# Kernel tuning notes

Measured on AMD Instinct MI355X. Metric: run time of the kernel, lower is better.

The kernel has to match this reference:

```python
import jax, jax.numpy as jnp
import numpy as np
jax.config.update("jax_enable_x64", True)  # match torch int64 hash wraparound

K = 4096  # codebook size
HASH_C = jnp.int64(73244475)


def mueller_hash(x):
    x = (x >> 16 ^ x) * HASH_C
    x = (x >> 16 ^ x) * HASH_C
    return x >> 16 ^ x


def fourier_act(x):
    # sin on even feature indices, cos on odd
    even = (jnp.arange(x.shape[-1]) % 2) == 0
    return jnp.where(even, jnp.sin(x), jnp.cos(x))


def setup_inputs() -> dict:
    key = jax.random.key(0)
    ks = jax.random.split(key, 10)
    f32 = jnp.float32
    N, D, H = 8192, 1024, 4096
    s = 0.02
    return {
        "x": jax.random.normal(ks[0], (N, D), dtype=f32),
        "w1": jax.random.normal(ks[1], (H, D), dtype=f32) * s,
        "b1": jnp.zeros((H,), dtype=f32),
        "w2": jax.random.normal(ks[2], (H, 2 * H), dtype=f32) * s,
        "b2": jnp.zeros((H,), dtype=f32),
        "w3": jax.random.normal(ks[3], (H, H), dtype=f32) * s,
        "b3": jnp.zeros((H,), dtype=f32),
        "w4": jax.random.normal(ks[4], (D, H), dtype=f32) * s,
        "b4": jnp.zeros((D,), dtype=f32),
        "emb": jax.random.normal(ks[5], (K, D), dtype=f32),
    }


def reference(x, w1, b1, w2, b2, w3, b3, w4, b4, emb):
    # FourierMLP
    h = x @ w1.T + b1                                  # [N, H]
    h = jnp.concatenate([h, fourier_act(h)], axis=-1)  # [N, 2H] (FourierAct cat=True)
    h = fourier_act(h @ w2.T + b2)                     # [N, H]
    h = fourier_act(h @ w3.T + b3)                     # [N, H]
    z = h @ w4.T + b4                                  # [N, D]

    # latent: cdist argmin == squared-distance argmin
    z2 = jnp.sum(z * z, axis=-1, keepdims=True)        # [N, 1]
    e2 = jnp.sum(emb * emb, axis=-1)                   # [K]
    d2 = z2 - 2.0 * (z @ emb.T) + e2                   # [N, K]
    idx = jnp.argmin(d2, axis=-1).astype(jnp.int64)    # [N]

    quantized = jnp.zeros_like(z)
    for i in range(1, 4):
        sel = mueller_hash(idx + jnp.int64(i * K)) & jnp.int64(K - 1)  # % K (K pow2)
        quantized = quantized + emb[sel] / 3.0
    return quantized
```

## Files before the change

kernel.cpp:

```cpp
#include <hip/hip_runtime.h>
#include <cstdint>

constexpr int NB = 8192;
constexpr int Dd = 1024;
constexpr int Hh = 4096;
constexpr int Kc = 4096;

using ull = unsigned long long;
typedef _Float16 half8 __attribute__((ext_vector_type(8)));
typedef float floatx16 __attribute__((ext_vector_type(16)));

#define TPB 256

__device__ __forceinline__ float fourier1(int col, float v) {
    return (col & 1) ? __cosf(v) : __sinf(v);
}

#define ASYNC_CP16(gp, sp)                                                          \
    __builtin_amdgcn_global_load_lds(                                               \
        (const __attribute__((address_space(1))) unsigned int*)(gp),                \
        (__attribute__((address_space(3))) unsigned int*)(sp), 16, 0, 0)

template<int MODE>
__global__ __launch_bounds__(TPB, 2)
void gemm_split(const _Float16* __restrict__ Agh, const _Float16* __restrict__ Agl,
                const _Float16* __restrict__ Bgh, const _Float16* __restrict__ Bgl,
                const float* __restrict__ bias, float invscale,
                _Float16* __restrict__ Ch, _Float16* __restrict__ Cl,
                int Kd, int ldc,
                const float* __restrict__ e2, ull* __restrict__ gkey)
{
    __shared__ _Float16 sAh[128 * 32];
    __shared__ _Float16 sAl[128 * 32];
    __shared__ _Float16 sBh[256 * 32];
    __shared__ _Float16 sBl[256 * 32];
    __shared__ ull red[256];

    const int tid = threadIdx.x, lane = tid & 63;
    const int w = tid >> 6;
    const int bn = blockIdx.x, bm = blockIdx.y;
    const int wm = w >> 1, wn = w & 1;
    const int l31 = lane & 31, lh = lane >> 5;

    size_t aoff[2], boff[4];
#pragma unroll
    for (int s = 0; s < 2; ++s) {
        int q = s * 256 + tid; int r = q >> 2;
        int c = (q & 3) ^ ((r >> 1) & 3);
        aoff[s] = (size_t)(bm * 128 + r) * Kd + c * 8;
    }
#pragma unroll
    for (int s = 0; s < 4; ++s) {
        int q = s * 256 + tid; int r = q >> 2;
        int c = (q & 3) ^ ((r >> 1) & 3);
        boff[s] = (size_t)(bn * 256 + r) * Kd + c * 8;
    }

    int arow[2], asw[2], brow[4], bsw[4];
#pragma unroll
    for (int mt = 0; mt < 2; ++mt) {
        int r = wm * 64 + mt * 32 + l31; arow[mt] = r * 32; asw[mt] = (r >> 1) & 3;
    }
#pragma unroll
    for (int nt = 0; nt < 4; ++nt) {
        int r = wn * 128 + nt * 32 + l31; brow[nt] = r * 32; bsw[nt] = (r >> 1) & 3;
    }

    floatx16 acc[2][4];
#pragma unroll
    for (int mt = 0; mt < 2; ++mt)
#pragma unroll
        for (int nt = 0; nt < 4; ++nt)
#pragma unroll
            for (int i = 0; i < 16; ++i) acc[mt][nt][i] = 0.f;

    for (int k0 = 0; k0 < Kd; k0 += 32) {
#pragma unroll
        for (int s = 0; s < 2; ++s) {
            ASYNC_CP16(Agh + aoff[s] + k0, sAh + (s * 256 + tid) * 8);
            ASYNC_CP16(Agl + aoff[s] + k0, sAl + (s * 256 + tid) * 8);
        }
#pragma unroll
        for (int s = 0; s < 4; ++s) {
            ASYNC_CP16(Bgh + boff[s] + k0, sBh + (s * 256 + tid) * 8);
            ASYNC_CP16(Bgl + boff[s] + k0, sBl + (s * 256 + tid) * 8);
        }
        __syncthreads();

#pragma unroll
        for (int kk = 0; kk < 2; ++kk) {
            const int ck = kk * 2 + lh;
            half8 ah[2], al[2], bh[4], bl[4];
#pragma unroll
            for (int mt = 0; mt < 2; ++mt) {
                int off = arow[mt] + (ck ^ asw[mt]) * 8;
                ah[mt] = *(const half8*)(sAh + off);
                al[mt] = *(const half8*)(sAl + off);
            }
#pragma unroll
            for (int nt = 0; nt < 4; ++nt) {
                int off = brow[nt] + (ck ^ bsw[nt]) * 8;
                bh[nt] = *(const half8*)(sBh + off);
                bl[nt] = *(const half8*)(sBl + off);
            }
#pragma unroll
            for (int mt = 0; mt < 2; ++mt)
#pragma unroll
                for (int nt = 0; nt < 4; ++nt)
                    acc[mt][nt] = __builtin_amdgcn_mfma_f32_32x32x16_f16(ah[mt], bh[nt], acc[mt][nt], 0, 0, 0);
#pragma unroll
            for (int mt = 0; mt < 2; ++mt)
#pragma unroll
                for (int nt = 0; nt < 4; ++nt)
                    acc[mt][nt] = __builtin_amdgcn_mfma_f32_32x32x16_f16(ah[mt], bl[nt], acc[mt][nt], 0, 0, 0);
#pragma unroll
            for (int mt = 0; mt < 2; ++mt)
#pragma unroll
                for (int nt = 0; nt < 4; ++nt)
                    acc[mt][nt] = __builtin_amdgcn_mfma_f32_32x32x16_f16(al[mt], bh[nt], acc[mt][nt], 0, 0, 0);
        }
        __syncthreads();
    }

    if (MODE != 3) {
        float bs[4];
#pragma unroll
        for (int nt = 0; nt < 4; ++nt) bs[nt] = bias[bn * 256 + wn * 128 + nt * 32 + l31];
#pragma unroll
        for (int mt = 0; mt < 2; ++mt) {
#pragma unroll
            for (int nt = 0; nt < 4; ++nt) {
                const int col = bn * 256 + wn * 128 + nt * 32 + l31;
#pragma unroll
                for (int r = 0; r < 16; ++r) {
                    const int mrow = (r & 3) + 8 * (r >> 2) + 4 * lh;
                    const size_t row = (size_t)(bm * 128 + wm * 64 + mt * 32 + mrow);
                    const float v = acc[mt][nt][r] * invscale + bs[nt];
                    const size_t o = row * ldc + col;
                    if (MODE == 0) {
                        _Float16 h = (_Float16)v;
                        Ch[o] = h; Cl[o] = (_Float16)(v - (float)h);
                    } else if (MODE == 1) {
                        float f = fourier1(col, v);
                        _Float16 h = (_Float16)f;
                        Ch[o] = h; Cl[o] = (_Float16)(f - (float)h);
                    } else {
                        _Float16 h = (_Float16)v;
                        Ch[o] = h; Cl[o] = (_Float16)(v - (float)h);
                        float f = fourier1(col, v);
                        _Float16 hf = (_Float16)f;
                        Ch[o + Hh] = hf; Cl[o + Hh] = (_Float16)(f - (float)hf);
                    }
                }
            }
        }
    } else {
        float es[4];
#pragma unroll
        for (int nt = 0; nt < 4; ++nt) es[nt] = e2[bn * 256 + wn * 128 + nt * 32 + l31];
#pragma unroll
        for (int mt = 0; mt < 2; ++mt) {
#pragma unroll
            for (int r = 0; r < 16; ++r) {
                ull best = ~0ull;
#pragma unroll
                for (int nt = 0; nt < 4; ++nt) {
                    const int col = bn * 256 + wn * 128 + nt * 32 + l31;
                    float sc = es[nt] - 2.0f * acc[mt][nt][r];
                    unsigned u = __float_as_uint(sc);
                    u = (u & 0x80000000u) ? ~u : (u | 0x80000000u);
                    ull key = ((ull)u << 32) | (unsigned)col;
                    best = best < key ? best : key;
                }
#pragma unroll
                for (int m = 16; m >= 1; m >>= 1) {
                    ull o = __shfl_xor(best, m, 64);
                    best = best < o ? best : o;
                }
                if (l31 == 0) {
                    int rl = wm * 64 + mt * 32 + (r & 3) + 8 * (r >> 2) + 4 * lh;
                    red[rl * 2 + wn] = best;
                }
            }
        }
        __syncthreads();
        if (tid < 128) {
            ull a = red[tid * 2], b = red[tid * 2 + 1];
            atomicMin(&gkey[(size_t)bm * 128 + tid], a < b ? a : b);
        }
    }
}

__global__ void split_f16(const float* __restrict__ src, _Float16* __restrict__ hi,
                          _Float16* __restrict__ lo, int n8, float scale)
{
    int i = blockIdx.x * blockDim.x + threadIdx.x;
    if (i >= n8) return;
    const float4* s4 = (const float4*)src;
    float4 v0 = s4[i * 2], v1 = s4[i * 2 + 1];
    float v[8] = {v0.x, v0.y, v0.z, v0.w, v1.x, v1.y, v1.z, v1.w};
    half8 h, l;
#pragma unroll
    for (int j = 0; j < 8; ++j) {
        float x = v[j] * scale;
        _Float16 hh = (_Float16)x;
        h[j] = hh;
        l[j] = (_Float16)(x - (float)hh);
    }
    *(half8*)(hi + (size_t)i * 8) = h;
    *(half8*)(lo + (size_t)i * 8) = l;
}

__global__ void init_gkey(ull* gkey) {
    int i = blockIdx.x * blockDim.x + threadIdx.x;
    if (i < NB) gkey[i] = ~0ull;
}

__global__ void e2_kernel(const float* __restrict__ emb, float* __restrict__ e2) {
    int k = blockIdx.x, t = threadIdx.x;
    float s = 0.f;
    for (int d = t; d < Dd; d += 256) {
        float v = emb[(size_t)k * Dd + d];
        s += v * v;
    }
    __shared__ float r[256];
    r[t] = s; __syncthreads();
    for (int off = 128; off > 0; off >>= 1) {
        if (t < off) r[t] += r[t + off];
        __syncthreads();
    }
    if (t == 0) e2[k] = r[0];
}

__device__ __forceinline__ long long mueller(long long x) {
    x = (long long)((unsigned long long)(x ^ (x >> 16)) * 73244475ull);
    x = (long long)((unsigned long long)(x ^ (x >> 16)) * 73244475ull);
    return x ^ (x >> 16);
}

__global__ void out_kernel(const float* __restrict__ emb,
                           const ull* __restrict__ gkey,
                           float* __restrict__ out) {
    const int n = blockIdx.x;
    const int t = threadIdx.x;
    long long idx = (long long)(unsigned)(gkey[n] & 0xFFFFFFFFull);
    int s1 = (int)(mueller(idx + 1LL * Kc) & (long long)(Kc - 1));
    int s2 = (int)(mueller(idx + 2LL * Kc) & (long long)(Kc - 1));
    int s3 = (int)(mueller(idx + 3LL * Kc) & (long long)(Kc - 1));
    const float* e1p = emb + (size_t)s1 * Dd;
    const float* e2p = emb + (size_t)s2 * Dd;
    const float* e3p = emb + (size_t)s3 * Dd;
    float* op = out + (size_t)n * Dd;
    for (int d = t; d < Dd; d += 256)
        op[d] = e1p[d] / 3.0f + e2p[d] / 3.0f + e3p[d] / 3.0f;
}

__device__ __forceinline__ float fourier1p(int col, float v) {
    return (col & 1) ? cosf(v) : sinf(v);
}

template<int MODE>
__global__ __launch_bounds__(TPB)
void gemm_tn(const float* __restrict__ A, const float* __restrict__ B,
             const float* __restrict__ bias, float* __restrict__ C,
             int Kd, int ldc)
{
    __shared__ float As[16][132];
    __shared__ float Bs[16][132];
    const int t  = threadIdx.x;
    const int bn = blockIdx.x, bm = blockIdx.y;
    const int rowL = t >> 2;
    const int kq   = t & 3;
    const int rm   = (t >> 4) << 3;
    const int rn   = (t & 15) << 3;

    const float* Ab = A + (size_t)(bm * 128 + rowL) * Kd + kq * 4;
    const float* Bb = B + (size_t)(bn * 128 + rowL) * Kd + kq * 4;
    const size_t strideHalf = (size_t)64 * Kd;

    float acc[8][8];
#pragma unroll
    for (int i = 0; i < 8; ++i)
#pragma unroll
        for (int j = 0; j < 8; ++j) acc[i][j] = 0.f;

    for (int k0 = 0; k0 < Kd; k0 += 16) {
        float4 a0 = *(const float4*)(Ab + k0);
        float4 a1 = *(const float4*)(Ab + strideHalf + k0);
        float4 b0 = *(const float4*)(Bb + k0);
        float4 b1 = *(const float4*)(Bb + strideHalf + k0);
        __syncthreads();
        As[kq*4+0][rowL]    = a0.x; As[kq*4+1][rowL]    = a0.y;
        As[kq*4+2][rowL]    = a0.z; As[kq*4+3][rowL]    = a0.w;
        As[kq*4+0][rowL+64] = a1.x; As[kq*4+1][rowL+64] = a1.y;
        As[kq*4+2][rowL+64] = a1.z; As[kq*4+3][rowL+64] = a1.w;
        Bs[kq*4+0][rowL]    = b0.x; Bs[kq*4+1][rowL]    = b0.y;
        Bs[kq*4+2][rowL]    = b0.z; Bs[kq*4+3][rowL]    = b0.w;
        Bs[kq*4+0][rowL+64] = b1.x; Bs[kq*4+1][rowL+64] = b1.y;
        Bs[kq*4+2][rowL+64] = b1.z; Bs[kq*4+3][rowL+64] = b1.w;
        __syncthreads();
#pragma unroll
        for (int kk = 0; kk < 16; ++kk) {
            float4 av0 = *(const float4*)&As[kk][rm];
            float4 av1 = *(const float4*)&As[kk][rm + 4];
            float4 bv0 = *(const float4*)&Bs[kk][rn];
            float4 bv1 = *(const float4*)&Bs[kk][rn + 4];
            float a[8] = {av0.x, av0.y, av0.z, av0.w, av1.x, av1.y, av1.z, av1.w};
            float b[8] = {bv0.x, bv0.y, bv0.z, bv0.w, bv1.x, bv1.y, bv1.z, bv1.w};
#pragma unroll
            for (int i = 0; i < 8; ++i)
#pragma unroll
                for (int j = 0; j < 8; ++j)
                    acc[i][j] = fmaf(a[i], b[j], acc[i][j]);
        }
    }

    const int gm = bm * 128 + rm;
    const int gn = bn * 128 + rn;
#pragma unroll
    for (int i = 0; i < 8; ++i) {
#pragma unroll
        for (int j = 0; j < 8; ++j) {
            float v = acc[i][j] + bias[gn + j];
            size_t o = (size_t)(gm + i) * ldc + (gn + j);
            if (MODE == 0) {
                C[o] = v;
            } else if (MODE == 1) {
                C[o] = fourier1p(gn + j, v);
            } else {
                C[o]      = v;
                C[o + Hh] = fourier1p(gn + j, v);
            }
        }
    }
}

__global__ __launch_bounds__(TPB)
void dist_argmin(const float* __restrict__ Z, const float* __restrict__ E,
                 const float* __restrict__ e2, ull* __restrict__ gkey)
{
    __shared__ float As[16][132];
    __shared__ float Bs[16][132];
    __shared__ ull   red[128][16];
    const int t  = threadIdx.x;
    const int bn = blockIdx.x, bm = blockIdx.y;
    const int rowL = t >> 2;
    const int kq   = t & 3;
    const int rm   = (t >> 4) << 3;
    const int rn   = (t & 15) << 3;
    const int Kd = Dd;

    const float* Ab = Z + (size_t)(bm * 128 + rowL) * Kd + kq * 4;
    const float* Bb = E + (size_t)(bn * 128 + rowL) * Kd + kq * 4;
    const size_t strideHalf = (size_t)64 * Kd;

    float acc[8][8];
#pragma unroll
    for (int i = 0; i < 8; ++i)
#pragma unroll
        for (int j = 0; j < 8; ++j) acc[i][j] = 0.f;

    for (int k0 = 0; k0 < Kd; k0 += 16) {
        float4 a0 = *(const float4*)(Ab + k0);
        float4 a1 = *(const float4*)(Ab + strideHalf + k0);
        float4 b0 = *(const float4*)(Bb + k0);
        float4 b1 = *(const float4*)(Bb + strideHalf + k0);
        __syncthreads();
        As[kq*4+0][rowL]    = a0.x; As[kq*4+1][rowL]    = a0.y;
        As[kq*4+2][rowL]    = a0.z; As[kq*4+3][rowL]    = a0.w;
        As[kq*4+0][rowL+64] = a1.x; As[kq*4+1][rowL+64] = a1.y;
        As[kq*4+2][rowL+64] = a1.z; As[kq*4+3][rowL+64] = a1.w;
        Bs[kq*4+0][rowL]    = b0.x; Bs[kq*4+1][rowL]    = b0.y;
        Bs[kq*4+2][rowL]    = b0.z; Bs[kq*4+3][rowL]    = b0.w;
        Bs[kq*4+0][rowL+64] = b1.x; Bs[kq*4+1][rowL+64] = b1.y;
        Bs[kq*4+2][rowL+64] = b1.z; Bs[kq*4+3][rowL+64] = b1.w;
        __syncthreads();
#pragma unroll
        for (int kk = 0; kk < 16; ++kk) {
            float4 av0 = *(const float4*)&As[kk][rm];
            float4 av1 = *(const float4*)&As[kk][rm + 4];
            float4 bv0 = *(const float4*)&Bs[kk][rn];
            float4 bv1 = *(const float4*)&Bs[kk][rn + 4];
            float a[8] = {av0.x, av0.y, av0.z, av0.w, av1.x, av1.y, av1.z, av1.w};
            float b[8] = {bv0.x, bv0.y, bv0.z, bv0.w, bv1.x, bv1.y, bv1.z, bv1.w};
#pragma unroll
            for (int i = 0; i < 8; ++i)
#pragma unroll
                for (int j = 0; j < 8; ++j)
                    acc[i][j] = fmaf(a[i], b[j], acc[i][j]);
        }
    }

    const int gn = bn * 128 + rn;
#pragma unroll
    for (int i = 0; i < 8; ++i) {
        ull best = ~0ull;
#pragma unroll
        for (int j = 0; j < 8; ++j) {
            int gk = gn + j;
            float sc = e2[gk] - 2.0f * acc[i][j];
            unsigned u = __float_as_uint(sc);
            u = (u & 0x80000000u) ? ~u : (u | 0x80000000u);
            ull key = ((ull)u << 32) | (unsigned)gk;
            best = best < key ? best : key;
        }
        red[rm + i][t & 15] = best;
    }
    __syncthreads();
    if (t < 128) {
        ull m = red[t][0];
#pragma unroll
        for (int q = 1; q < 16; ++q) m = m < red[t][q] ? m : red[t][q];
        atomicMin(&gkey[(size_t)bm * 128 + t], m);
    }
}

extern "C" void kernel_launch(void* const* d_in, const int* in_sizes, int n_in,
                              void* d_out, int out_size, void* d_ws, size_t ws_size,
                              hipStream_t stream) {
    const float* x   = (const float*)d_in[0];
    const float* w1  = (const float*)d_in[1];
    const float* b1  = (const float*)d_in[2];
    const float* w2  = (const float*)d_in[3];
    const float* b2  = (const float*)d_in[4];
    const float* w3  = (const float*)d_in[5];
    const float* b3  = (const float*)d_in[6];
    const float* w4  = (const float*)d_in[7];
    const float* b4  = (const float*)d_in[8];
    const float* emb = (const float*)d_in[9];
    float* out = (float*)d_out;

    const size_t MB = 1024 * 1024;

    if (ws_size >= 512 * MB) {
        char* W = (char*)d_ws;
        _Float16* hcat_h = (_Float16*)(W);
        _Float16* hcat_l = (_Float16*)(W + 128 * MB);
        _Float16* w3h = (_Float16*)(W);
        _Float16* w3l = (_Float16*)(W + 32 * MB);
        _Float16* w4h = (_Float16*)(W + 64 * MB);
        _Float16* w4l = (_Float16*)(W + 72 * MB);
        _Float16* eh  = (_Float16*)(W + 80 * MB);
        _Float16* el  = (_Float16*)(W + 88 * MB);
        float*    e2b = (float*)   (W + 96 * MB);
        ull*      gkey = (ull*)    (W + 96 * MB + 16 * 1024);
        _Float16* w2h = (_Float16*)(W + 256 * MB);
        _Float16* w2l = (_Float16*)(W + 320 * MB);
        _Float16* h3h = (_Float16*)(W + 256 * MB);
        _Float16* h3l = (_Float16*)(W + 320 * MB);
        _Float16* xh  = (_Float16*)(W + 384 * MB);
        _Float16* xl  = (_Float16*)(W + 400 * MB);
        _Float16* w1h = (_Float16*)(W + 416 * MB);
        _Float16* w1l = (_Float16*)(W + 424 * MB);
        _Float16* h2h = (_Float16*)(W + 384 * MB);
        _Float16* h2l = (_Float16*)(W + 448 * MB);
        _Float16* zh  = (_Float16*)d_out;
        _Float16* zl  = zh + (size_t)NB * Dd;

        const float WS = 64.0f, IWS = 1.0f / 64.0f;

        split_f16<<<dim3(1048576 / 256), 256, 0, stream>>>(x,  xh,  xl,  1048576, 1.0f);
        split_f16<<<dim3(524288  / 256), 256, 0, stream>>>(w1, w1h, w1l, 524288,  WS);
        split_f16<<<dim3(4194304 / 256), 256, 0, stream>>>(w2, w2h, w2l, 4194304, WS);

        gemm_split<2><<<dim3(Hh / 256, NB / 128), TPB, 0, stream>>>(
            xh, xl, w1h, w1l, b1, IWS, hcat_h, hcat_l, Dd, 2 * Hh, nullptr, nullptr);
        gemm_split<1><<<dim3(Hh / 256, NB / 128), TPB, 0, stream>>>(
            hcat_h, hcat_l, w2h, w2l, b2, IWS, h2h, h2l, 2 * Hh, Hh, nullptr, nullptr);

        split_f16<<<dim3(2097152 / 256), 256, 0, stream>>>(w3,  w3h, w3l, 2097152, WS);
        split_f16<<<dim3(524288  / 256), 256, 0, stream>>>(w4,  w4h, w4l, 524288,  WS);
        split_f16<<<dim3(524288  / 256), 256, 0, stream>>>(emb, eh,  el,  524288,  1.0f);
        e2_kernel<<<dim3(Kc), dim3(256), 0, stream>>>(emb, e2b);
        init_gkey<<<dim3(NB / 256), dim3(256), 0, stream>>>(gkey);

        gemm_split<1><<<dim3(Hh / 256, NB / 128), TPB, 0, stream>>>(
            h2h, h2l, w3h, w3l, b3, IWS, h3h, h3l, Hh, Hh, nullptr, nullptr);
        gemm_split<0><<<dim3(Dd / 256, NB / 128), TPB, 0, stream>>>(
            h3h, h3l, w4h, w4l, b4, IWS, zh, zl, Hh, Dd, nullptr, nullptr);
        gemm_split<3><<<dim3(Kc / 256, NB / 128), TPB, 0, stream>>>(
            zh, zl, eh, el, nullptr, 1.0f, nullptr, nullptr, Dd, 0, e2b, gkey);

        out_kernel<<<dim3(NB), dim3(256), 0, stream>>>(emb, gkey, out);
    } else {
        float* hcat  = (float*)d_ws;
        float* h2    = hcat + (size_t)NB * 2 * Hh;
        float* e2buf = h2 + (size_t)NB * Hh;
        ull*   gkey  = (ull*)(e2buf + Kc);
        float* h3    = hcat;

        init_gkey<<<dim3((NB + 255) / 256), dim3(256), 0, stream>>>(gkey);
        e2_kernel<<<dim3(Kc), dim3(256), 0, stream>>>(emb, e2buf);
        gemm_tn<2><<<dim3(Hh / 128, NB / 128), TPB, 0, stream>>>(x, w1, b1, hcat, Dd, 2 * Hh);
        gemm_tn<1><<<dim3(Hh / 128, NB / 128), TPB, 0, stream>>>(hcat, w2, b2, h2, 2 * Hh, Hh);
        gemm_tn<1><<<dim3(Hh / 128, NB / 128), TPB, 0, stream>>>(h2, w3, b3, h3, Hh, Hh);
        gemm_tn<0><<<dim3(Dd / 128, NB / 128), TPB, 0, stream>>>(h3, w4, b4, out, Hh, Dd);
        dist_argmin<<<dim3(Kc / 128, NB / 128), TPB, 0, stream>>>(out, emb, e2buf, gkey);
        out_kernel<<<dim3(NB), dim3(256), 0, stream>>>(emb, gkey, out);
    }
}
```

Before: 3.698 ms.

## Store GEMM A operand in MFMA fragment layout and load it directly to registers

Activations are now written by each GEMM epilogue, and by a new split kernel for x, in a pre-tiled layout that matches the 32x32x16 MFMA A-fragment order. The GEMM then reads A straight from global memory into registers with one contiguous 16-byte load per lane, dropping the A shared-memory tiles and their LDS reads. This is meant to cut LDS traffic and shared-memory footprint in the main loop. In exchange, the two waves that share an A tile each fetch it from global or L2 separately, and the A loads are not double-buffered, so their latency may be exposed.

```diff
diff --git a/kernel.cpp b/kernel.cpp
--- a/kernel.cpp
+++ b/kernel.cpp
@@ -20,6 +20,7 @@
     __builtin_amdgcn_global_load_lds(                                               \
         (const __attribute__((address_space(1))) unsigned int*)(gp),                \
         (__attribute__((address_space(3))) unsigned int*)(sp), 16, 0, 0)
+
 
 template<int MODE>
 __global__ __launch_bounds__(TPB, 2)
@@ -30,8 +31,6 @@
                 int Kd, int ldc,
                 const float* __restrict__ e2, ull* __restrict__ gkey)
 {
-    __shared__ _Float16 sAh[128 * 32];
-    __shared__ _Float16 sAl[128 * 32];
     __shared__ _Float16 sBh[256 * 32];
     __shared__ _Float16 sBl[256 * 32];
     __shared__ ull red[256];
@@ -41,14 +40,9 @@
     const int bn = blockIdx.x, bm = blockIdx.y;
     const int wm = w >> 1, wn = w & 1;
     const int l31 = lane & 31, lh = lane >> 5;
-
-    size_t aoff[2], boff[4];
-#pragma unroll
-    for (int s = 0; s < 2; ++s) {
-        int q = s * 256 + tid; int r = q >> 2;
-        int c = (q & 3) ^ ((r >> 1) & 3);
-        aoff[s] = (size_t)(bm * 128 + r) * Kd + c * 8;
-    }
+    const int kpf = Kd >> 4;
+
+    size_t boff[4];
 #pragma unroll
     for (int s = 0; s < 4; ++s) {
         int q = s * 256 + tid; int r = q >> 2;
@@ -56,16 +50,17 @@
         boff[s] = (size_t)(bn * 256 + r) * Kd + c * 8;
     }
 
-    int arow[2], asw[2], brow[4], bsw[4];
-#pragma unroll
-    for (int mt = 0; mt < 2; ++mt) {
-        int r = wm * 64 + mt * 32 + l31; arow[mt] = r * 32; asw[mt] = (r >> 1) & 3;
-    }
+    int brow[4], bsw[4];
 #pragma unroll
     for (int nt = 0; nt < 4; ++nt) {
         int r = wn * 128 + nt * 32 + l31; brow[nt] = r * 32; bsw[nt] = (r >> 1) & 3;
     }
 
+    size_t abase[2];
+#pragma unroll
+    for (int mt = 0; mt < 2; ++mt)
+        abase[mt] = (size_t)(bm * 4 + wm * 2 + mt) * kpf * 512 + (size_t)lane * 8;
+
     floatx16 acc[2][4];
 #pragma unroll
     for (int mt = 0; mt < 2; ++mt)
@@ -74,29 +69,27 @@
 #pragma unroll
             for (int i = 0; i < 16; ++i) acc[mt][nt][i] = 0.f;
 
-    for (int k0 = 0; k0 < Kd; k0 += 32) {
-#pragma unroll
-        for (int s = 0; s < 2; ++s) {
-            ASYNC_CP16(Agh + aoff[s] + k0, sAh + (s * 256 + tid) * 8);
-            ASYNC_CP16(Agl + aoff[s] + k0, sAl + (s * 256 + tid) * 8);
-        }
+    for (int k0 = 0, ki = 0; k0 < Kd; k0 += 32, ki += 2) {
 #pragma unroll
         for (int s = 0; s < 4; ++s) {
             ASYNC_CP16(Bgh + boff[s] + k0, sBh + (s * 256 + tid) * 8);
             ASYNC_CP16(Bgl + boff[s] + k0, sBl + (s * 256 + tid) * 8);
         }
+        half8 ahr[2][2], alr[2][2];
+#pragma unroll
+        for (int kk = 0; kk < 2; ++kk)
+#pragma unroll
+            for (int mt = 0; mt < 2; ++mt) {
+                size_t o = abase[mt] + (size_t)(ki + kk) * 512;
+                ahr[kk][mt] = *(const half8*)(Agh + o);
+                alr[kk][mt] = *(const half8*)(Agl + o);
+            }
         __syncthreads();
 
 #pragma unroll
         for (int kk = 0; kk < 2; ++kk) {
             const int ck = kk * 2 + lh;
-            half8 ah[2], al[2], bh[4], bl[4];
-#pragma unroll
-            for (int mt = 0; mt < 2; ++mt) {
-                int off = arow[mt] + (ck ^ asw[mt]) * 8;
-                ah[mt] = *(const half8*)(sAh + off);
-                al[mt] = *(const half8*)(sAl + off);
-            }
+            half8 bh[4], bl[4];
 #pragma unroll
             for (int nt = 0; nt < 4; ++nt) {
                 int off = brow[nt] + (ck ^ bsw[nt]) * 8;
@@ -107,36 +100,39 @@
             for (int mt = 0; mt < 2; ++mt)
 #pragma unroll
                 for (int nt = 0; nt < 4; ++nt)
-                    acc[mt][nt] = __builtin_amdgcn_mfma_f32_32x32x16_f16(ah[mt], bh[nt], acc[mt][nt], 0, 0, 0);
+                    acc[mt][nt] = __builtin_amdgcn_mfma_f32_32x32x16_f16(ahr[kk][mt], bh[nt], acc[mt][nt], 0, 0, 0);
 #pragma unroll
             for (int mt = 0; mt < 2; ++mt)
 #pragma unroll
                 for (int nt = 0; nt < 4; ++nt)
-                    acc[mt][nt] = __builtin_amdgcn_mfma_f32_32x32x16_f16(ah[mt], bl[nt], acc[mt][nt], 0, 0, 0);
+                    acc[mt][nt] = __builtin_amdgcn_mfma_f32_32x32x16_f16(ahr[kk][mt], bl[nt], acc[mt][nt], 0, 0, 0);
 #pragma unroll
             for (int mt = 0; mt < 2; ++mt)
 #pragma unroll
                 for (int nt = 0; nt < 4; ++nt)
-                    acc[mt][nt] = __builtin_amdgcn_mfma_f32_32x32x16_f16(al[mt], bh[nt], acc[mt][nt], 0, 0, 0);
+                    acc[mt][nt] = __builtin_amdgcn_mfma_f32_32x32x16_f16(alr[kk][mt], bh[nt], acc[mt][nt], 0, 0, 0);
         }
         __syncthreads();
     }
 
     if (MODE != 3) {
+        const int kpo = ldc >> 4;
         float bs[4];
 #pragma unroll
         for (int nt = 0; nt < 4; ++nt) bs[nt] = bias[bn * 256 + wn * 128 + nt * 32 + l31];
 #pragma unroll
         for (int mt = 0; mt < 2; ++mt) {
+            const size_t rowblk = (size_t)(bm * 4 + wm * 2 + mt) * kpo;
 #pragma unroll
             for (int nt = 0; nt < 4; ++nt) {
                 const int col = bn * 256 + wn * 128 + nt * 32 + l31;
+                const size_t fb  = (rowblk + (col >> 4)) * 512 + ((col >> 3) & 1) * 256 + (col & 7);
+                const size_t fb2 = fb + (size_t)256 * 512;
 #pragma unroll
                 for (int r = 0; r < 16; ++r) {
                     const int mrow = (r & 3) + 8 * (r >> 2) + 4 * lh;
-                    const size_t row = (size_t)(bm * 128 + wm * 64 + mt * 32 + mrow);
                     const float v = acc[mt][nt][r] * invscale + bs[nt];
-                    const size_t o = row * ldc + col;
+                    const size_t o = fb + mrow * 8;
                     if (MODE == 0) {
                         _Float16 h = (_Float16)v;
                         Ch[o] = h; Cl[o] = (_Float16)(v - (float)h);
@@ -149,7 +145,7 @@
                         Ch[o] = h; Cl[o] = (_Float16)(v - (float)h);
                         float f = fourier1(col, v);
                         _Float16 hf = (_Float16)f;
-                        Ch[o + Hh] = hf; Cl[o + Hh] = (_Float16)(f - (float)hf);
+                        Ch[fb2 + mrow * 8] = hf; Cl[fb2 + mrow * 8] = (_Float16)(f - (float)hf);
                     }
                 }
             }
@@ -203,6 +199,31 @@
 #pragma unroll
     for (int j = 0; j < 8; ++j) {
         float x = v[j] * scale;
+        _Float16 hh = (_Float16)x;
+        h[j] = hh;
+        l[j] = (_Float16)(x - (float)hh);
+    }
+    *(half8*)(hi + (size_t)i * 8) = h;
+    *(half8*)(lo + (size_t)i * 8) = l;
+}
+
+__global__ void split_f16_frag(const float* __restrict__ src, _Float16* __restrict__ hi,
+                               _Float16* __restrict__ lo, int n8, int Kd)
+{
+    int i = blockIdx.x * blockDim.x + threadIdx.x;
+    if (i >= n8) return;
+    int e = i * 8;
+    int f = e >> 9;
+    int ww = e & 511;
+    int khalf = ww >> 8, row32 = (ww >> 3) & 31;
+    int kpf = Kd >> 4;
+    int rowblk = f / kpf, kch = f - rowblk * kpf;
+    int m = rowblk * 32 + row32, k = kch * 16 + khalf * 8;
+    const float* s = src + (size_t)m * Kd + k;
+    half8 h, l;
+#pragma unroll
+    for (int j = 0; j < 8; ++j) {
+        float x = s[j];
         _Float16 hh = (_Float16)x;
         h[j] = hh;
         l[j] = (_Float16)(x - (float)hh);
@@ -459,7 +480,7 @@
 
         const float WS = 64.0f, IWS = 1.0f / 64.0f;
 
-        split_f16<<<dim3(1048576 / 256), 256, 0, stream>>>(x,  xh,  xl,  1048576, 1.0f);
+        split_f16_frag<<<dim3(1048576 / 256), 256, 0, stream>>>(x, xh, xl, 1048576, Dd);
         split_f16<<<dim3(524288  / 256), 256, 0, stream>>>(w1, w1h, w1l, 524288,  WS);
         split_f16<<<dim3(4194304 / 256), 256, 0, stream>>>(w2, w2h, w2l, 4194304, WS);
 
```

New measurement: 3.366 ms. 1.1x faster.
